# Kernel optimization log

Hardware: AMD Instinct MI355X
Metric: run time of the kernel (lower is better)

## Reference

```python
import jax, jax.numpy as jnp
import numpy as np

NUM_CLASSES = 16  # foreground classes 1..16; 0 = background (ignored, as in the torch loop)
EPS = 1e-8       # F.cosine_similarity default eps


def setup_inputs() -> dict:
    key = jax.random.key(0)
    k1, k2, k3 = jax.random.split(key, 3)
    B, C, H, W = 8, 1024, 64, 64
    support_features = jax.random.normal(k1, (B, C, H, W), dtype=jnp.float32)
    support_masks = jax.random.randint(k2, (B, 1, H, W), 0, NUM_CLASSES + 1, dtype=jnp.int32)
    query_features = jax.random.normal(k3, (B, C, H, W), dtype=jnp.float32)
    return {
        "support_features": support_features,
        "support_masks": support_masks,
        "query_features": query_features,
    }


def reference(support_features, support_masks, query_features):
    B, C, H, W = query_features.shape
    K = NUM_CLASSES
    # --- compute_prototypes: masked spatial mean per class ---
    classes = jnp.arange(1, K + 1, dtype=support_masks.dtype)           # (K,)
    m = (support_masks[:, 0][:, None] == classes[None, :, None, None])  # (B,K,H,W) bool
    m = m.astype(support_features.dtype)
    num = jnp.einsum('bchw,bkhw->bkc', support_features, m)             # (B,K,C)
    den = m.sum(axis=(2, 3))[:, :, None]                                # (B,K,1)
    prototypes = num / den                                              # (B,K,C)
    # --- match_prototypes: cosine similarity + argmax over classes ---
    q = query_features.reshape(B, C, H * W)                             # (B,C,P)
    dots = jnp.einsum('bkc,bcp->bkp', prototypes, q)                    # (B,K,P)
    qn = jnp.linalg.norm(q, axis=1)                                     # (B,P)
    pn = jnp.linalg.norm(prototypes, axis=2)                            # (B,K)
    sims = dots / jnp.maximum(pn[:, :, None] * qn[:, None, :], EPS)     # (B,K,P)
    segmentation_map = jnp.argmax(sims, axis=1).reshape(B, H, W)
    return segmentation_map
```

## Files before the change

kernel.cpp:

```cpp
#include <hip/hip_runtime.h>
#include <math.h>

#define BB 8
#define CC 1024
#define PP 4096
#define KK 16
#define EPSF 1e-8f


__global__ __launch_bounds__(256) void k_num(const float* __restrict__ sf,
                                             const int* __restrict__ sm,
                                             float* __restrict__ num) {
    int blk  = blockIdx.x;
    int b    = blk >> 7;
    int cg   = blk & 127;
    int wave = threadIdx.x >> 6;
    int lane = threadIdx.x & 63;
    int c0   = cg * 8 + wave * 2;

    const float* f0 = sf + ((size_t)b * CC + c0) * PP;
    const float* f1 = f0 + PP;
    const int*   m  = sm + (size_t)b * PP;

    float a0[KK], a1[KK];
#pragma unroll
    for (int k = 0; k < KK; ++k) { a0[k] = 0.f; a1[k] = 0.f; }

    for (int it = 0; it < PP / 64; ++it) {
        int p   = it * 64 + lane;
        int mv  = m[p];
        float v0 = f0[p];
        float v1 = f1[p];
#pragma unroll
        for (int k = 0; k < KK; ++k) {
            float pr = (mv == k + 1) ? 1.0f : 0.0f;
            a0[k] = fmaf(pr, v0, a0[k]);
            a1[k] = fmaf(pr, v1, a1[k]);
        }
    }

#pragma unroll
    for (int k = 0; k < KK; ++k) {
#pragma unroll
        for (int s = 32; s >= 1; s >>= 1) {
            a0[k] += __shfl_xor(a0[k], s, 64);
            a1[k] += __shfl_xor(a1[k], s, 64);
        }
    }

    if (lane == 0) {
        float* o = num + (size_t)b * KK * CC + c0;
#pragma unroll
        for (int k = 0; k < KK; ++k) {
            o[(size_t)k * CC]     = a0[k];
            o[(size_t)k * CC + 1] = a1[k];
        }
    }
}

__global__ __launch_bounds__(256) void k_den(const int* __restrict__ sm,
                                             float* __restrict__ den) {
    int b    = blockIdx.x;
    int tid  = threadIdx.x;
    int wave = tid >> 6;
    int lane = tid & 63;
    const int* m = sm + (size_t)b * PP;

    float cnt[KK];
#pragma unroll
    for (int k = 0; k < KK; ++k) cnt[k] = 0.f;

    for (int it = 0; it < PP / 256; ++it) {
        int mv = m[it * 256 + tid];
#pragma unroll
        for (int k = 0; k < KK; ++k) cnt[k] += (mv == k + 1) ? 1.0f : 0.0f;
    }

#pragma unroll
    for (int k = 0; k < KK; ++k) {
#pragma unroll
        for (int s = 32; s >= 1; s >>= 1) cnt[k] += __shfl_xor(cnt[k], s, 64);
    }

    __shared__ float wsum[4][KK];
    if (lane == 0) {
#pragma unroll
        for (int k = 0; k < KK; ++k) wsum[wave][k] = cnt[k];
    }
    __syncthreads();
    if (tid < KK)
        den[b * KK + tid] = wsum[0][tid] + wsum[1][tid] + wsum[2][tid] + wsum[3][tid];
}

__global__ __launch_bounds__(256) void k_proto(const float* __restrict__ num,
                                               const float* __restrict__ den,
                                               float* __restrict__ proto_t,
                                               float* __restrict__ pn) {
    int b   = blockIdx.x >> 4;
    int k   = blockIdx.x & 15;
    int tid = threadIdx.x;
    const float* nu = num + ((size_t)b * KK + k) * CC;
    float d = den[b * KK + k];

    float sq = 0.f;
#pragma unroll
    for (int i = 0; i < CC / 256; ++i) {
        int c = i * 256 + tid;
        float pv = nu[c] / d;
        proto_t[((size_t)b * CC + c) * KK + k] = pv;
        sq = fmaf(pv, pv, sq);
    }

#pragma unroll
    for (int s = 32; s >= 1; s >>= 1) sq += __shfl_xor(sq, s, 64);

    __shared__ float red[4];
    if ((tid & 63) == 0) red[tid >> 6] = sq;
    __syncthreads();
    if (tid == 0) pn[b * KK + k] = sqrtf(red[0] + red[1] + red[2] + red[3]);
}

__global__ __launch_bounds__(256) void k_match(const float* __restrict__ qf,
                                               const float* __restrict__ proto_t,
                                               const float* __restrict__ pn,
                                               int* __restrict__ out) {
    int b    = blockIdx.x >> 6;
    int pg   = blockIdx.x & 63;
    int tid  = threadIdx.x;
    int lane = tid & 63;
    int chunk = __builtin_amdgcn_readfirstlane(tid >> 6);
    int px   = pg * 64 + lane;

    const float* q  = qf + ((size_t)b * CC + (size_t)chunk * 256) * PP + px;
    const float* pt = proto_t + ((size_t)b * CC + (size_t)chunk * 256) * KK;

    float dot[KK];
#pragma unroll
    for (int k = 0; k < KK; ++k) dot[k] = 0.f;
    float qs = 0.f;

    for (int ci = 0; ci < 256; ++ci) {
        float qv = q[(size_t)ci * PP];
        const float* pr = pt + ci * KK;
#pragma unroll
        for (int k = 0; k < KK; ++k) dot[k] = fmaf(pr[k], qv, dot[k]);
        qs = fmaf(qv, qv, qs);
    }

    __shared__ float red[4][64][KK + 1];
#pragma unroll
    for (int k = 0; k < KK; ++k) red[chunk][lane][k] = dot[k];
    red[chunk][lane][KK] = qs;
    __syncthreads();

    if (tid < 64) {
        float q2 = red[0][tid][KK] + red[1][tid][KK] + red[2][tid][KK] + red[3][tid][KK];
        float qn = sqrtf(q2);
        float bv = -INFINITY;
        int   bi = 0;
#pragma unroll
        for (int k = 0; k < KK; ++k) {
            float dk = red[0][tid][k] + red[1][tid][k] + red[2][tid][k] + red[3][tid][k];
            float s  = dk / fmaxf(pn[b * KK + k] * qn, EPSF);
            if (s > bv) { bv = s; bi = k; }
        }
        out[(size_t)b * PP + pg * 64 + tid] = bi;
    }
}

extern "C" void kernel_launch(void* const* d_in, const int* in_sizes, int n_in,
                              void* d_out, int out_size, void* d_ws, size_t ws_size,
                              hipStream_t stream) {
    const float* sf = (const float*)d_in[0];
    const int*   sm = (const int*)d_in[1];
    const float* qf = (const float*)d_in[2];
    int* out = (int*)d_out;

    char*  ws      = (char*)d_ws;
    float* num     = (float*)(ws);
    float* den     = (float*)(ws + (512u << 10));
    float* pn      = (float*)(ws + (512u << 10) + 512);
    float* proto_t = (float*)(ws + (1u << 20));

    hipLaunchKernelGGL(k_num,   dim3(1024), dim3(256), 0, stream, sf, sm, num);
    hipLaunchKernelGGL(k_den,   dim3(8),    dim3(256), 0, stream, sm, den);
    hipLaunchKernelGGL(k_proto, dim3(128),  dim3(256), 0, stream, num, den, proto_t, pn);
    hipLaunchKernelGGL(k_match, dim3(512),  dim3(256), 0, stream, qf, proto_t, pn, out);
}
```

Measured before the change: 309.8 us.

## Vectorize loads in prototype and matching kernels, transpose num layout, widen match blocks

k_num now reads features and masks as float4/int4 and writes num in a (b,c,k) layout with float4 stores, so k_proto can read and write coalesced with one block per batch. k_match uses 512-thread blocks over 8 channel chunks, with each lane handling two pixels via float2 loads, and reduces the partial sums through a two-stage shared-memory tree. The aim is fewer, wider memory transactions and more reuse of each prototype load. k_proto drops from 128 to 8 blocks, which may underutilize the GPU for that small step.

After: 320.9 us. +3.6%, slower.

```diff
diff --git a/kernel.cpp b/kernel.cpp
--- a/kernel.cpp
+++ b/kernel.cpp
@@ -11,32 +11,38 @@
 __global__ __launch_bounds__(256) void k_num(const float* __restrict__ sf,
                                              const int* __restrict__ sm,
                                              float* __restrict__ num) {
-    int blk  = blockIdx.x;
-    int b    = blk >> 7;
-    int cg   = blk & 127;
-    int wave = threadIdx.x >> 6;
+    int b    = blockIdx.x >> 7;
+    int cg   = blockIdx.x & 127;
+    int w    = threadIdx.x >> 6;
     int lane = threadIdx.x & 63;
-    int c0   = cg * 8 + wave * 2;
-
-    const float* f0 = sf + ((size_t)b * CC + c0) * PP;
-    const float* f1 = f0 + PP;
-    const int*   m  = sm + (size_t)b * PP;
+    int c0   = cg * 8 + w * 2;
+
+    const float4* f0 = (const float4*)(sf + ((size_t)b * CC + c0) * PP);
+    const float4* f1 = (const float4*)(sf + ((size_t)b * CC + c0 + 1) * PP);
+    const int4*   m4 = (const int4*)(sm + (size_t)b * PP);
 
     float a0[KK], a1[KK];
 #pragma unroll
     for (int k = 0; k < KK; ++k) { a0[k] = 0.f; a1[k] = 0.f; }
 
-    for (int it = 0; it < PP / 64; ++it) {
-        int p   = it * 64 + lane;
-        int mv  = m[p];
-        float v0 = f0[p];
-        float v1 = f1[p];
-#pragma unroll
-        for (int k = 0; k < KK; ++k) {
-            float pr = (mv == k + 1) ? 1.0f : 0.0f;
-            a0[k] = fmaf(pr, v0, a0[k]);
-            a1[k] = fmaf(pr, v1, a1[k]);
-        }
+    for (int it = 0; it < PP / 256; ++it) {
+        int p = it * 64 + lane;
+        int4   mv = m4[p];
+        float4 v0 = f0[p];
+        float4 v1 = f1[p];
+
+        auto px = [&](int m_, float x0, float x1) {
+#pragma unroll
+            for (int k = 0; k < KK; ++k) {
+                float pr = (m_ == k + 1) ? 1.0f : 0.0f;
+                a0[k] = fmaf(pr, x0, a0[k]);
+                a1[k] = fmaf(pr, x1, a1[k]);
+            }
+        };
+        px(mv.x, v0.x, v1.x);
+        px(mv.y, v0.y, v1.y);
+        px(mv.z, v0.z, v1.z);
+        px(mv.w, v0.w, v1.w);
     }
 
 #pragma unroll
@@ -49,11 +55,12 @@
     }
 
     if (lane == 0) {
-        float* o = num + (size_t)b * KK * CC + c0;
-#pragma unroll
-        for (int k = 0; k < KK; ++k) {
-            o[(size_t)k * CC]     = a0[k];
-            o[(size_t)k * CC + 1] = a1[k];
+        float4* o0 = (float4*)(num + ((size_t)b * CC + c0) * KK);
+        float4* o1 = (float4*)(num + ((size_t)b * CC + c0 + 1) * KK);
+#pragma unroll
+        for (int g = 0; g < 4; ++g) {
+            o0[g] = make_float4(a0[4*g], a0[4*g+1], a0[4*g+2], a0[4*g+3]);
+            o1[g] = make_float4(a1[4*g], a1[4*g+1], a1[4*g+2], a1[4*g+3]);
         }
     }
 }
@@ -96,75 +103,102 @@
                                                const float* __restrict__ den,
                                                float* __restrict__ proto_t,
                                                float* __restrict__ pn) {
-    int b   = blockIdx.x >> 4;
-    int k   = blockIdx.x & 15;
+    int b   = blockIdx.x;
     int tid = threadIdx.x;
-    const float* nu = num + ((size_t)b * KK + k) * CC;
+    int k   = tid & 15;
+    int cs  = tid >> 4;
     float d = den[b * KK + k];
 
     float sq = 0.f;
-#pragma unroll
-    for (int i = 0; i < CC / 256; ++i) {
-        int c = i * 256 + tid;
-        float pv = nu[c] / d;
-        proto_t[((size_t)b * CC + c) * KK + k] = pv;
+    for (int c = cs; c < CC; c += 16) {
+        size_t idx = ((size_t)b * CC + c) * KK + k;
+        float pv = num[idx] / d;
+        proto_t[idx] = pv;
         sq = fmaf(pv, pv, sq);
     }
 
-#pragma unroll
-    for (int s = 32; s >= 1; s >>= 1) sq += __shfl_xor(sq, s, 64);
-
-    __shared__ float red[4];
-    if ((tid & 63) == 0) red[tid >> 6] = sq;
-    __syncthreads();
-    if (tid == 0) pn[b * KK + k] = sqrtf(red[0] + red[1] + red[2] + red[3]);
-}
-
-__global__ __launch_bounds__(256) void k_match(const float* __restrict__ qf,
+    sq += __shfl_xor(sq, 16, 64);
+    sq += __shfl_xor(sq, 32, 64);
+    __shared__ float red[4][KK];
+    if ((tid & 63) < KK) red[tid >> 6][k] = sq;
+    __syncthreads();
+    if (tid < KK)
+        pn[b * KK + tid] = sqrtf(red[0][tid] + red[1][tid] + red[2][tid] + red[3][tid]);
+}
+
+__global__ __launch_bounds__(512) void k_match(const float* __restrict__ qf,
                                                const float* __restrict__ proto_t,
                                                const float* __restrict__ pn,
                                                int* __restrict__ out) {
-    int b    = blockIdx.x >> 6;
-    int pg   = blockIdx.x & 63;
+    int b    = blockIdx.x >> 5;
+    int pg   = blockIdx.x & 31;
     int tid  = threadIdx.x;
     int lane = tid & 63;
-    int chunk = __builtin_amdgcn_readfirstlane(tid >> 6);
-    int px   = pg * 64 + lane;
-
-    const float* q  = qf + ((size_t)b * CC + (size_t)chunk * 256) * PP + px;
-    const float* pt = proto_t + ((size_t)b * CC + (size_t)chunk * 256) * KK;
-
-    float dot[KK];
-#pragma unroll
-    for (int k = 0; k < KK; ++k) dot[k] = 0.f;
-    float qs = 0.f;
-
-    for (int ci = 0; ci < 256; ++ci) {
-        float qv = q[(size_t)ci * PP];
+    int w    = __builtin_amdgcn_readfirstlane(tid >> 6);
+    int c0   = w * 128;
+    int px0  = pg * 128;
+
+    const float2* q2 = (const float2*)(qf + ((size_t)b * CC + c0) * PP + px0);
+    const float*  pt = proto_t + ((size_t)b * CC + c0) * KK;
+
+    float2 dot[KK];
+#pragma unroll
+    for (int k = 0; k < KK; ++k) { dot[k].x = 0.f; dot[k].y = 0.f; }
+    float2 qs; qs.x = 0.f; qs.y = 0.f;
+
+    for (int ci = 0; ci < 128; ++ci) {
+        float2 qv = q2[(size_t)ci * (PP / 2) + lane];
         const float* pr = pt + ci * KK;
 #pragma unroll
-        for (int k = 0; k < KK; ++k) dot[k] = fmaf(pr[k], qv, dot[k]);
-        qs = fmaf(qv, qv, qs);
-    }
-
-    __shared__ float red[4][64][KK + 1];
-#pragma unroll
-    for (int k = 0; k < KK; ++k) red[chunk][lane][k] = dot[k];
-    red[chunk][lane][KK] = qs;
-    __syncthreads();
-
-    if (tid < 64) {
-        float q2 = red[0][tid][KK] + red[1][tid][KK] + red[2][tid][KK] + red[3][tid][KK];
-        float qn = sqrtf(q2);
+        for (int k = 0; k < KK; ++k) {
+            float p = pr[k];
+            dot[k].x = fmaf(p, qv.x, dot[k].x);
+            dot[k].y = fmaf(p, qv.y, dot[k].y);
+        }
+        qs.x = fmaf(qv.x, qv.x, qs.x);
+        qs.y = fmaf(qv.y, qv.y, qs.y);
+    }
+
+    __shared__ float2 buf[4][KK + 1][64];
+
+    if (w >= 4) {
+#pragma unroll
+        for (int k = 0; k < KK; ++k) buf[w - 4][k][lane] = dot[k];
+        buf[w - 4][KK][lane] = qs;
+    }
+    __syncthreads();
+    if (w < 4) {
+#pragma unroll
+        for (int k = 0; k < KK; ++k) {
+            float2 t = buf[w][k][lane];
+            t.x += dot[k].x; t.y += dot[k].y;
+            buf[w][k][lane] = t;
+        }
+        float2 t = buf[w][KK][lane];
+        t.x += qs.x; t.y += qs.y;
+        buf[w][KK][lane] = t;
+    }
+    __syncthreads();
+
+    if (tid < 128) {
+        int px = tid;
+        const float* bf = (const float*)buf;
+        float q2s = 0.f;
+#pragma unroll
+        for (int c = 0; c < 4; ++c) q2s += bf[((c * (KK + 1)) + KK) * 128 + px];
+        float qn = sqrtf(q2s);
+
         float bv = -INFINITY;
         int   bi = 0;
 #pragma unroll
         for (int k = 0; k < KK; ++k) {
-            float dk = red[0][tid][k] + red[1][tid][k] + red[2][tid][k] + red[3][tid][k];
-            float s  = dk / fmaxf(pn[b * KK + k] * qn, EPSF);
+            float dk = 0.f;
+#pragma unroll
+            for (int c = 0; c < 4; ++c) dk += bf[((c * (KK + 1)) + k) * 128 + px];
+            float s = dk / fmaxf(pn[b * KK + k] * qn, EPSF);
             if (s > bv) { bv = s; bi = k; }
         }
-        out[(size_t)b * PP + pg * 64 + tid] = bi;
+        out[(size_t)b * PP + px0 + px] = bi;
     }
 }
 
@@ -184,6 +218,6 @@
 
     hipLaunchKernelGGL(k_num,   dim3(1024), dim3(256), 0, stream, sf, sm, num);
     hipLaunchKernelGGL(k_den,   dim3(8),    dim3(256), 0, stream, sm, den);
-    hipLaunchKernelGGL(k_proto, dim3(128),  dim3(256), 0, stream, num, den, proto_t, pn);
-    hipLaunchKernelGGL(k_match, dim3(512),  dim3(256), 0, stream, qf, proto_t, pn, out);
-}
+    hipLaunchKernelGGL(k_proto, dim3(8),    dim3(256), 0, stream, num, den, proto_t, pn);
+    hipLaunchKernelGGL(k_match, dim3(256),  dim3(512), 0, stream, qf, proto_t, pn, out);
+}
```
